# Kernel optimization log

Hardware: AMD Instinct MI355X
Metric: run time of the kernel (lower is better)

Reference implementation:

```python
import jax, jax.numpy as jnp
import numpy as np

HIDDEN = 2048
INTER = 768
N_EXPERTS = 64
TOP_K = 8
BATCH, SEQ = 2, 2048


def setup_inputs() -> dict:
    key = jax.random.key(0)
    k_x, k_g, k_gp, k_up, k_dp = jax.random.split(key, 5)
    s_in = 1.0 / np.sqrt(HIDDEN)   # lecun_normal fan_in scaling
    s_mid = 1.0 / np.sqrt(INTER)
    return {
        "x": jax.random.normal(k_x, (BATCH, SEQ, HIDDEN), dtype=jnp.float32),
        "gate_w": jax.random.normal(k_g, (HIDDEN, N_EXPERTS), dtype=jnp.float32) * s_in,
        "gate_proj": jax.random.normal(k_gp, (N_EXPERTS, HIDDEN, INTER), dtype=jnp.float32) * s_in,
        "up_proj": jax.random.normal(k_up, (N_EXPERTS, HIDDEN, INTER), dtype=jnp.float32) * s_in,
        "down_proj": jax.random.normal(k_dp, (N_EXPERTS, INTER, HIDDEN), dtype=jnp.float32) * s_mid,
    }


def reference(x, gate_w, gate_proj, up_proj, down_proj):
    H = x.shape[-1]
    E = gate_proj.shape[0]
    K = TOP_K

    x_flat = x.reshape(-1, H)                      # [T, H]
    router_logits = x_flat @ gate_w                # [T, E]

    routing_weights, selected_experts = jax.lax.top_k(router_logits, k=K)  # [T, K]
    routing_weights = jax.nn.softmax(routing_weights, axis=-1)

    sel_flat = jnp.ravel(selected_experts)         # [T*K]
    x_expanded = jnp.repeat(x_flat, K, axis=0)     # [T*K, H]

    sort_idx = jnp.argsort(sel_flat)
    unsort_idx = jnp.argsort(sort_idx)
    x_sorted = x_expanded[sort_idx]                # tokens grouped by expert
    group_sizes = jnp.bincount(sel_flat, length=E)

    gate_out = jax.lax.ragged_dot(x_sorted, gate_proj, group_sizes)  # [T*K, I]
    up_out = jax.lax.ragged_dot(x_sorted, up_proj, group_sizes)      # [T*K, I]
    activated = jax.nn.silu(gate_out) * up_out
    down_out = jax.lax.ragged_dot(activated, down_proj, group_sizes)  # [T*K, H]

    unsorted = down_out[unsort_idx].reshape(-1, K, H)  # [T, K, H]
    out = (unsorted * routing_weights[..., None]).sum(axis=1)
    return out.reshape(x.shape), router_logits
```

## Files before the change

kernel.cpp:

```cpp
#include <hip/hip_runtime.h>
#include <hip/hip_bf16.h>
#include <cstdint>

#define NTOK 4096
#define HID  2048
#define ITER 768
#define NEXP 64
#define TOPK 8
#define MAXT 320

typedef __attribute__((ext_vector_type(8))) short sh8;
typedef __attribute__((ext_vector_type(4))) float f32x4;

#define MFMA16 __builtin_amdgcn_mfma_f32_16x16x32_bf16

__device__ __forceinline__ uint16_t f2b(float f) {
  union { float f; uint32_t u; } v; v.f = f;
  uint32_t u = v.u;
  u += 0x7FFFu + ((u >> 16) & 1u);
  return (uint16_t)(u >> 16);
}

__device__ __forceinline__ float b2f_lo(uint32_t w) {
  union { uint32_t u; float f; } v; v.u = w << 16; return v.f;
}
__device__ __forceinline__ float b2f_hi(uint32_t w) {
  union { uint32_t u; float f; } v; v.u = w & 0xffff0000u; return v.f;
}

__device__ __forceinline__ uint32_t cvtpk(float lo, float hi) {
  float2 f2; f2.x = lo; f2.y = hi;
  __hip_bfloat162 h = __float22bfloat162_rn(f2);
  union { __hip_bfloat162 h; uint32_t u; } v; v.h = h;
  return v.u;
}

__device__ __forceinline__ void gl2lds16(const void* g, void* l) {
  __builtin_amdgcn_global_load_lds(
      (const __attribute__((address_space(1))) uint32_t*)g,
      (__attribute__((address_space(3))) uint32_t*)l, 16, 0, 0);
}

__device__ __forceinline__ int xcd_unswizzle(int s, int na) {
  int q = na >> 3, r = na & 7, x = s & 7, i = s >> 3;
  return (x < r ? x * (q + 1) : r * (q + 1) + (x - r) * q) + i;
}

__global__ void zero_kernel(int* __restrict__ cc) {
  cc[threadIdx.x] = 0;
}

__global__ __launch_bounds__(256) void xcast_kernel(const float* __restrict__ x,
                                                    uint16_t* __restrict__ xb) {
  size_t i = ((size_t)blockIdx.x * 256 + threadIdx.x) * 8;
  float4 a = *(const float4*)(x + i);
  float4 b = *(const float4*)(x + i + 4);
  uint4 o;
  o.x = (uint32_t)f2b(a.x) | ((uint32_t)f2b(a.y) << 16);
  o.y = (uint32_t)f2b(a.z) | ((uint32_t)f2b(a.w) << 16);
  o.z = (uint32_t)f2b(b.x) | ((uint32_t)f2b(b.y) << 16);
  o.w = (uint32_t)f2b(b.z) | ((uint32_t)f2b(b.w) << 16);
  *(uint4*)(xb + i) = o;
}

__global__ __launch_bounds__(256) void router_kernel(
    const float* __restrict__ x, const float* __restrict__ gate_w,
    float* __restrict__ logits, int* __restrict__ topk_id,
    float* __restrict__ topk_w, int* __restrict__ counts)
{
  int lane = threadIdx.x & 63;
  int wv   = threadIdx.x >> 6;
  int t    = blockIdx.x * 4 + wv;
  const float* xr = x + (size_t)t * HID;
  float acc = 0.f;
  #pragma unroll 4
  for (int h = 0; h < HID; h += 4) {
    float4 xv = *(const float4*)(xr + h);
    acc += xv.x * gate_w[(h + 0) * NEXP + lane];
    acc += xv.y * gate_w[(h + 1) * NEXP + lane];
    acc += xv.z * gate_w[(h + 2) * NEXP + lane];
    acc += xv.w * gate_w[(h + 3) * NEXP + lane];
  }
  logits[(size_t)t * NEXP + lane] = acc;

  float v = acc;
  float topv[TOPK]; int topi[TOPK];
  #pragma unroll
  for (int k = 0; k < TOPK; ++k) {
    float bv = v; int bi = lane;
    #pragma unroll
    for (int off = 32; off > 0; off >>= 1) {
      float ov = __shfl_xor(bv, off);
      int   oi = __shfl_xor(bi, off);
      if (ov > bv || (ov == bv && oi < bi)) { bv = ov; bi = oi; }
    }
    topv[k] = bv; topi[k] = bi;
    if (lane == bi) v = -3.0e38f;
  }
  float m = topv[0], s = 0.f, w[TOPK];
  #pragma unroll
  for (int k = 0; k < TOPK; ++k) { w[k] = __expf(topv[k] - m); s += w[k]; }
  float inv = 1.f / s;
  if (lane < TOPK) {
    topk_id[t * TOPK + lane] = topi[lane];
    topk_w[t * TOPK + lane]  = w[lane] * inv;
    atomicAdd(&counts[topi[lane]], 1);
  }
}

__global__ void offsets_kernel(const int* __restrict__ counts, int* __restrict__ offsets,
                               int* __restrict__ tiles, int* __restrict__ tilecount) {
  if (threadIdx.x == 0) {
    int s = 0, nt = 0;
    for (int e = 0; e < NEXP; ++e) {
      offsets[e] = s;
      int c = counts[e];
      for (int rb = 0; rb * 128 < c; ++rb) tiles[nt++] = (e << 16) | rb;
      s += c;
    }
    offsets[NEXP] = s;
    tilecount[0] = nt;
  }
}

__global__ __launch_bounds__(256) void scatter_kernel(
    const int* __restrict__ topk_id,
    const int* __restrict__ offsets, int* __restrict__ cursor,
    int* __restrict__ pair_tok, int* __restrict__ inv)
{
  int p = blockIdx.x * 256 + threadIdx.x;
  int e = topk_id[p];
  int pos = offsets[e] + atomicAdd(&cursor[e], 1);
  pair_tok[pos] = p;
  inv[p] = pos;
}

__global__ __launch_bounds__(256, 2) void gateup_kernel(
    const uint16_t* __restrict__ xb,
    const float* __restrict__ gate_proj,
    const float* __restrict__ up_proj,
    const int* __restrict__ pair_tok,
    const int* __restrict__ offsets,
    const int* __restrict__ tiles,
    const int* __restrict__ tilecount,
    uint16_t* __restrict__ act)
{
  const int nt = tilecount[0];
  const int na = nt * 12;
  if (blockIdx.x >= na) return;
  const int L  = xcd_unswizzle(blockIdx.x, na);
  const int ti = L % nt, nc = L / nt;
  const int te = tiles[ti];
  const int e = te >> 16, row0 = (te & 0xffff) * 128;
  const int start = offsets[e];
  const int count = offsets[e + 1] - start;
  const int nvalid = min(128, count - row0);

  __shared__ __align__(16) uint16_t aT[2 * 128 * 64];
  __shared__ __align__(16) uint16_t bT[128 * 64];
  __shared__ int s_tok[128];

  const int t = threadIdx.x, l = t & 63, w = t >> 6;
  if (t < 128)
    s_tok[t] = (t < nvalid) ? (pair_tok[start + row0 + t] >> 3) : 0;
  __syncthreads();

  const int sub = l >> 3;
  const int xk  = ((l & 7) ^ sub) << 3;
  const uint16_t* srcA[4]; char* dstA[4];
  #pragma unroll
  for (int q = 0; q < 4; ++q) {
    int rl = (w * 4 + q) * 8 + sub;
    srcA[q] = xb + (size_t)s_tok[rl] * HID + xk;
    dstA[q] = (char*)aT + (w * 4 + q) * 1024;
  }

  const int brow = t & 127;
  const int kk0  = (t >> 7) * 32;
  const int rcomb  = nc * 128 + brow;
  const int n_orig = ((rcomb >> 5) << 4) + (rcomb & 15);
  const int is_up  = (rcomb >> 4) & 1;
  const float* wsrc = (is_up ? up_proj : gate_proj)
                    + (size_t)e * HID * ITER + n_orig;
  uint16_t* bwr[4];
  #pragma unroll
  for (int s = 0; s < 4; ++s) {
    int kb = (kk0 * 2 + 16 * s) ^ ((brow & 7) << 4);
    bwr[s] = (uint16_t*)((char*)bT + brow * 128 + kb);
  }

  const int wr = w >> 1, wc = w & 1, lr = l & 15, hi = l >> 4;
  const int xorv = (lr & 7) << 4;

  f32x4 acc[4][4];
  #pragma unroll
  for (int mi = 0; mi < 4; ++mi)
    #pragma unroll
    for (int ni = 0; ni < 4; ++ni)
      acc[mi][ni] = (f32x4){0.f, 0.f, 0.f, 0.f};

  float va[32];
  {
    const float* wp = wsrc + (size_t)kk0 * ITER;
    #pragma unroll
    for (int j = 0; j < 32; ++j) va[j] = wp[(size_t)j * ITER];
  }
  #pragma unroll
  for (int q = 0; q < 4; ++q)
    gl2lds16(srcA[q], dstA[q]);

  for (int kc = 0; kc < 32; ++kc) {
    __syncthreads();
    #pragma unroll
    for (int s = 0; s < 4; ++s) {
      uint4 o;
      o.x = cvtpk(va[s * 8 + 0], va[s * 8 + 1]);
      o.y = cvtpk(va[s * 8 + 2], va[s * 8 + 3]);
      o.z = cvtpk(va[s * 8 + 4], va[s * 8 + 5]);
      o.w = cvtpk(va[s * 8 + 6], va[s * 8 + 7]);
      *(uint4*)bwr[s] = o;
    }
    __syncthreads();
    if (kc + 1 < 32) {
      const float* wp = wsrc + (size_t)((kc + 1) * 64 + kk0) * ITER;
      #pragma unroll
      for (int j = 0; j < 32; ++j) va[j] = wp[(size_t)j * ITER];
      #pragma unroll
      for (int q = 0; q < 4; ++q)
        gl2lds16(srcA[q] + (kc + 1) * 64, dstA[q] + ((kc + 1) & 1) * 16384);
    }
    __builtin_amdgcn_sched_barrier(0);
    const char* aBuf = (const char*)aT + (kc & 1) * 16384;
    #pragma unroll
    for (int ks = 0; ks < 2; ++ks) {
      sh8 af[4], bf[4];
      #pragma unroll
      for (int mi = 0; mi < 4; ++mi)
        af[mi] = *(const sh8*)(aBuf +
                   (wr * 64 + mi * 16 + lr) * 128 + ((ks * 64 + hi * 16) ^ xorv));
      #pragma unroll
      for (int ni = 0; ni < 4; ++ni)
        bf[ni] = *(const sh8*)((const char*)bT +
                   (wc * 64 + ni * 16 + lr) * 128 + ((ks * 64 + hi * 16) ^ xorv));
      #pragma unroll
      for (int mi = 0; mi < 4; ++mi)
        #pragma unroll
        for (int ni = 0; ni < 4; ++ni)
          acc[mi][ni] = MFMA16(af[mi], bf[ni], acc[mi][ni], 0, 0, 0);
    }
  }

  #pragma unroll
  for (int mi = 0; mi < 4; ++mi)
    #pragma unroll
    for (int p = 0; p < 2; ++p)
      #pragma unroll
      for (int j = 0; j < 4; ++j) {
        int row = wr * 64 + mi * 16 + hi * 4 + j;
        if (row < nvalid) {
          float g = acc[mi][2 * p][j], u = acc[mi][2 * p + 1][j];
          float a = (g / (1.f + __expf(-g))) * u;
          int col = nc * 64 + wc * 32 + p * 16 + lr;
          act[(size_t)(start + row0 + row) * ITER + col] = f2b(a);
        }
      }
}

__global__ __launch_bounds__(256, 2) void down_kernel(
    const uint16_t* __restrict__ act,
    const float* __restrict__ down_proj,
    const int* __restrict__ offsets,
    const int* __restrict__ tiles,
    const int* __restrict__ tilecount,
    uint16_t* __restrict__ dd)
{
  const int nt = tilecount[0];
  const int na = nt * 16;
  if (blockIdx.x >= na) return;
  const int L  = xcd_unswizzle(blockIdx.x, na);
  const int ti = L % nt, nc = L / nt;
  const int te = tiles[ti];
  const int e = te >> 16, row0 = (te & 0xffff) * 128;
  const int start = offsets[e];
  const int count = offsets[e + 1] - start;
  const int nvalid = min(128, count - row0);

  __shared__ __align__(16) uint16_t aT[2 * 128 * 64];
  __shared__ __align__(16) uint16_t bT[128 * 64];

  const int t = threadIdx.x, l = t & 63, w = t >> 6;

  const int sub = l >> 3;
  const int xk  = ((l & 7) ^ sub) << 3;

  const uint16_t* srcA[4]; char* dstA[4];
  #pragma unroll
  for (int q = 0; q < 4; ++q) {
    int rl = (w * 4 + q) * 8 + sub;
    srcA[q] = act + (size_t)(start + row0 + rl) * ITER + xk;
    dstA[q] = (char*)aT + (w * 4 + q) * 1024;
  }

  const int brow = t & 127;
  const int kk0  = (t >> 7) * 32;
  const float* wsrc = down_proj + (size_t)e * ITER * HID + nc * 128 + brow;
  uint16_t* bwr[4];
  #pragma unroll
  for (int s = 0; s < 4; ++s) {
    int kb = (kk0 * 2 + 16 * s) ^ ((brow & 7) << 4);
    bwr[s] = (uint16_t*)((char*)bT + brow * 128 + kb);
  }

  const int wr = w >> 1, wc = w & 1, lr = l & 15, hi = l >> 4;
  const int xorv = (lr & 7) << 4;

  f32x4 acc[4][4];
  #pragma unroll
  for (int mi = 0; mi < 4; ++mi)
    #pragma unroll
    for (int ni = 0; ni < 4; ++ni)
      acc[mi][ni] = (f32x4){0.f, 0.f, 0.f, 0.f};

  float va[32];
  {
    const float* wp = wsrc + (size_t)kk0 * HID;
    #pragma unroll
    for (int j = 0; j < 32; ++j) va[j] = wp[(size_t)j * HID];
  }
  #pragma unroll
  for (int q = 0; q < 4; ++q)
    gl2lds16(srcA[q], dstA[q]);

  for (int kc = 0; kc < 12; ++kc) {
    __syncthreads();
    #pragma unroll
    for (int s = 0; s < 4; ++s) {
      uint4 o;
      o.x = cvtpk(va[s * 8 + 0], va[s * 8 + 1]);
      o.y = cvtpk(va[s * 8 + 2], va[s * 8 + 3]);
      o.z = cvtpk(va[s * 8 + 4], va[s * 8 + 5]);
      o.w = cvtpk(va[s * 8 + 6], va[s * 8 + 7]);
      *(uint4*)bwr[s] = o;
    }
    __syncthreads();
    if (kc + 1 < 12) {
      const float* wp = wsrc + (size_t)((kc + 1) * 64 + kk0) * HID;
      #pragma unroll
      for (int j = 0; j < 32; ++j) va[j] = wp[(size_t)j * HID];
      #pragma unroll
      for (int q = 0; q < 4; ++q)
        gl2lds16(srcA[q] + (kc + 1) * 64, dstA[q] + ((kc + 1) & 1) * 16384);
    }
    __builtin_amdgcn_sched_barrier(0);
    const char* aBuf = (const char*)aT + (kc & 1) * 16384;
    #pragma unroll
    for (int ks = 0; ks < 2; ++ks) {
      sh8 af[4], bf[4];
      #pragma unroll
      for (int mi = 0; mi < 4; ++mi)
        af[mi] = *(const sh8*)(aBuf +
                   (wr * 64 + mi * 16 + lr) * 128 + ((ks * 64 + hi * 16) ^ xorv));
      #pragma unroll
      for (int ni = 0; ni < 4; ++ni)
        bf[ni] = *(const sh8*)((const char*)bT +
                   (wc * 64 + ni * 16 + lr) * 128 + ((ks * 64 + hi * 16) ^ xorv));
      #pragma unroll
      for (int mi = 0; mi < 4; ++mi)
        #pragma unroll
        for (int ni = 0; ni < 4; ++ni)
          acc[mi][ni] = MFMA16(af[mi], bf[ni], acc[mi][ni], 0, 0, 0);
    }
  }

  #pragma unroll
  for (int mi = 0; mi < 4; ++mi)
    #pragma unroll
    for (int ni = 0; ni < 4; ++ni)
      #pragma unroll
      for (int j = 0; j < 4; ++j) {
        int row = wr * 64 + mi * 16 + hi * 4 + j;
        if (row < nvalid) {
          int col = nc * 128 + wc * 64 + ni * 16 + lr;
          dd[(size_t)(start + row0 + row) * HID + col] = f2b(acc[mi][ni][j]);
        }
      }
}

__global__ __launch_bounds__(256) void reduce_kernel(
    const uint16_t* __restrict__ dd, const float* __restrict__ topk_w,
    const int* __restrict__ inv, float* __restrict__ out)
{
  const int tok = blockIdx.x;
  const int c   = threadIdx.x * 8;
  float acc[8] = {0.f, 0.f, 0.f, 0.f, 0.f, 0.f, 0.f, 0.f};
  #pragma unroll
  for (int k = 0; k < TOPK; ++k) {
    const int   pos = inv[tok * TOPK + k];
    const float wk  = topk_w[tok * TOPK + k];
    uint4 v = *(const uint4*)&dd[(size_t)pos * HID + c];
    acc[0] += wk * b2f_lo(v.x);  acc[1] += wk * b2f_hi(v.x);
    acc[2] += wk * b2f_lo(v.y);  acc[3] += wk * b2f_hi(v.y);
    acc[4] += wk * b2f_lo(v.z);  acc[5] += wk * b2f_hi(v.z);
    acc[6] += wk * b2f_lo(v.w);  acc[7] += wk * b2f_hi(v.w);
  }
  float4 o0 = {acc[0], acc[1], acc[2], acc[3]};
  float4 o1 = {acc[4], acc[5], acc[6], acc[7]};
  float* op = out + (size_t)tok * HID + c;
  *(float4*)op       = o0;
  *(float4*)(op + 4) = o1;
}

extern "C" void kernel_launch(void* const* d_in, const int* in_sizes, int n_in,
                              void* d_out, int out_size, void* d_ws, size_t ws_size,
                              hipStream_t stream) {
  const float* x         = (const float*)d_in[0];
  const float* gate_w    = (const float*)d_in[1];
  const float* gate_proj = (const float*)d_in[2];
  const float* up_proj   = (const float*)d_in[3];
  const float* down_proj = (const float*)d_in[4];

  float* out    = (float*)d_out;
  float* logits = out + (size_t)NTOK * HID;

  char* ws = (char*)d_ws;
  size_t off = 0;
  uint16_t* xb      = (uint16_t*)(ws + off); off += (size_t)NTOK * HID * 2;
  uint16_t* act     = (uint16_t*)(ws + off); off += (size_t)(NTOK * TOPK + 128) * ITER * 2;
  uint16_t* dd      = (uint16_t*)(ws + off); off += (size_t)(NTOK * TOPK + 128) * HID * 2;
  int*      topk_id = (int*)  (ws + off); off += (size_t)NTOK * TOPK * 4;
  float*    topk_w  = (float*)(ws + off); off += (size_t)NTOK * TOPK * 4;
  int*      counts  = (int*)  (ws + off); off += 256;
  int*      cursor  = (int*)  (ws + off); off += 256;
  int*      offsets = (int*)  (ws + off); off += 512;
  int*      tiles   = (int*)  (ws + off); off += MAXT * 4;
  int*      tilecount=(int*)  (ws + off); off += 256;
  int*      pair_tok= (int*)  (ws + off); off += (size_t)NTOK * TOPK * 4;
  int*      inv     = (int*)  (ws + off); off += (size_t)NTOK * TOPK * 4;

  zero_kernel   <<<1,    128, 0, stream>>>(counts);
  xcast_kernel  <<<4096, 256, 0, stream>>>(x, xb);
  router_kernel <<<1024, 256, 0, stream>>>(x, gate_w, logits, topk_id, topk_w, counts);
  offsets_kernel<<<1,    64,  0, stream>>>(counts, offsets, tiles, tilecount);
  scatter_kernel<<<128,  256, 0, stream>>>(topk_id, offsets, cursor, pair_tok, inv);

  gateup_kernel<<<MAXT * 12, 256, 0, stream>>>(xb, gate_proj, up_proj, pair_tok, offsets,
                                               tiles, tilecount, act);
  down_kernel  <<<MAXT * 16, 256, 0, stream>>>(act, down_proj, offsets,
                                               tiles, tilecount, dd);
  reduce_kernel<<<NTOK, 256, 0, stream>>>(dd, topk_w, inv, out);
}
```

Baseline: 889.6 us.

## Double-buffer weight tiles in LDS and pipeline loads two stages ahead

Both expert GEMM kernels now double-buffer the bf16 weight tile in LDS as well as the activation tile. The prologue preloads and converts stage 0 and prefetches stage 1 weights into registers. The main loop issues the next A tile, writes the converted next B tile, and starts global loads two stages ahead, then runs the MFMAs at raised priority. The two __syncthreads per iteration become one s_barrier with a partial vmcnt wait, so memory latency overlaps with compute. This doubles B-tile LDS use, which may lower occupancy, and the hand-written waitcnt must match the exact count of outstanding loads.

```diff
diff --git a/kernel.cpp b/kernel.cpp
--- a/kernel.cpp
+++ b/kernel.cpp
@@ -157,7 +157,7 @@
   const int nvalid = min(128, count - row0);
 
   __shared__ __align__(16) uint16_t aT[2 * 128 * 64];
-  __shared__ __align__(16) uint16_t bT[128 * 64];
+  __shared__ __align__(16) uint16_t bT[2 * 128 * 64];
   __shared__ int s_tok[128];
 
   const int t = threadIdx.x, l = t & 63, w = t >> 6;
@@ -201,16 +201,38 @@
 
   float va[32];
   {
-    const float* wp = wsrc + (size_t)kk0 * ITER;
-    #pragma unroll
-    for (int j = 0; j < 32; ++j) va[j] = wp[(size_t)j * ITER];
-  }
-  #pragma unroll
-  for (int q = 0; q < 4; ++q)
-    gl2lds16(srcA[q], dstA[q]);
+    const float* wp0 = wsrc + (size_t)kk0 * ITER;
+    float v0[32];
+    #pragma unroll
+    for (int j = 0; j < 32; ++j) v0[j] = wp0[(size_t)j * ITER];
+    #pragma unroll
+    for (int q = 0; q < 4; ++q) gl2lds16(srcA[q], dstA[q]);
+    __builtin_amdgcn_sched_barrier(0);
+    #pragma unroll
+    for (int s = 0; s < 4; ++s) {
+      uint4 o;
+      o.x = cvtpk(v0[s * 8 + 0], v0[s * 8 + 1]);
+      o.y = cvtpk(v0[s * 8 + 2], v0[s * 8 + 3]);
+      o.z = cvtpk(v0[s * 8 + 4], v0[s * 8 + 5]);
+      o.w = cvtpk(v0[s * 8 + 6], v0[s * 8 + 7]);
+      *(uint4*)bwr[s] = o;
+    }
+    __builtin_amdgcn_sched_barrier(0);
+    const float* wp1 = wsrc + (size_t)(64 + kk0) * ITER;
+    #pragma unroll
+    for (int j = 0; j < 32; ++j) va[j] = wp1[(size_t)j * ITER];
+    __builtin_amdgcn_sched_barrier(0);
+  }
+  asm volatile("s_waitcnt vmcnt(32) lgkmcnt(0)" ::: "memory");
+  __builtin_amdgcn_s_barrier();
 
   for (int kc = 0; kc < 32; ++kc) {
-    __syncthreads();
+    const int cur = kc & 1, nxt = cur ^ 1;
+    const int k1 = min(kc + 1, 31);
+    #pragma unroll
+    for (int q = 0; q < 4; ++q)
+      gl2lds16(srcA[q] + k1 * 64, dstA[q] + nxt * 16384);
+    __builtin_amdgcn_sched_barrier(0);
     #pragma unroll
     for (int s = 0; s < 4; ++s) {
       uint4 o;
@@ -218,19 +240,19 @@
       o.y = cvtpk(va[s * 8 + 2], va[s * 8 + 3]);
       o.z = cvtpk(va[s * 8 + 4], va[s * 8 + 5]);
       o.w = cvtpk(va[s * 8 + 6], va[s * 8 + 7]);
-      *(uint4*)bwr[s] = o;
-    }
-    __syncthreads();
-    if (kc + 1 < 32) {
-      const float* wp = wsrc + (size_t)((kc + 1) * 64 + kk0) * ITER;
+      *(uint4*)(bwr[s] + nxt * 8192) = o;
+    }
+    __builtin_amdgcn_sched_barrier(0);
+    const int k2 = min(kc + 2, 31);
+    {
+      const float* wp = wsrc + (size_t)(k2 * 64 + kk0) * ITER;
       #pragma unroll
       for (int j = 0; j < 32; ++j) va[j] = wp[(size_t)j * ITER];
-      #pragma unroll
-      for (int q = 0; q < 4; ++q)
-        gl2lds16(srcA[q] + (kc + 1) * 64, dstA[q] + ((kc + 1) & 1) * 16384);
-    }
-    __builtin_amdgcn_sched_barrier(0);
-    const char* aBuf = (const char*)aT + (kc & 1) * 16384;
+    }
+    __builtin_amdgcn_sched_barrier(0);
+    __builtin_amdgcn_s_setprio(1);
+    const char* aBuf = (const char*)aT + cur * 16384;
+    const char* bBuf = (const char*)bT + cur * 16384;
     #pragma unroll
     for (int ks = 0; ks < 2; ++ks) {
       sh8 af[4], bf[4];
@@ -240,7 +262,7 @@
                    (wr * 64 + mi * 16 + lr) * 128 + ((ks * 64 + hi * 16) ^ xorv));
       #pragma unroll
       for (int ni = 0; ni < 4; ++ni)
-        bf[ni] = *(const sh8*)((const char*)bT +
+        bf[ni] = *(const sh8*)(bBuf +
                    (wc * 64 + ni * 16 + lr) * 128 + ((ks * 64 + hi * 16) ^ xorv));
       #pragma unroll
       for (int mi = 0; mi < 4; ++mi)
@@ -248,6 +270,10 @@
         for (int ni = 0; ni < 4; ++ni)
           acc[mi][ni] = MFMA16(af[mi], bf[ni], acc[mi][ni], 0, 0, 0);
     }
+    __builtin_amdgcn_s_setprio(0);
+    __builtin_amdgcn_sched_barrier(0);
+    asm volatile("s_waitcnt vmcnt(32) lgkmcnt(0)" ::: "memory");
+    __builtin_amdgcn_s_barrier();
   }
 
   #pragma unroll
@@ -286,7 +312,7 @@
   const int nvalid = min(128, count - row0);
 
   __shared__ __align__(16) uint16_t aT[2 * 128 * 64];
-  __shared__ __align__(16) uint16_t bT[128 * 64];
+  __shared__ __align__(16) uint16_t bT[2 * 128 * 64];
 
   const int t = threadIdx.x, l = t & 63, w = t >> 6;
 
@@ -323,16 +349,38 @@
 
   float va[32];
   {
-    const float* wp = wsrc + (size_t)kk0 * HID;
-    #pragma unroll
-    for (int j = 0; j < 32; ++j) va[j] = wp[(size_t)j * HID];
-  }
-  #pragma unroll
-  for (int q = 0; q < 4; ++q)
-    gl2lds16(srcA[q], dstA[q]);
+    const float* wp0 = wsrc + (size_t)kk0 * HID;
+    float v0[32];
+    #pragma unroll
+    for (int j = 0; j < 32; ++j) v0[j] = wp0[(size_t)j * HID];
+    #pragma unroll
+    for (int q = 0; q < 4; ++q) gl2lds16(srcA[q], dstA[q]);
+    __builtin_amdgcn_sched_barrier(0);
+    #pragma unroll
+    for (int s = 0; s < 4; ++s) {
+      uint4 o;
+      o.x = cvtpk(v0[s * 8 + 0], v0[s * 8 + 1]);
+      o.y = cvtpk(v0[s * 8 + 2], v0[s * 8 + 3]);
+      o.z = cvtpk(v0[s * 8 + 4], v0[s * 8 + 5]);
+      o.w = cvtpk(v0[s * 8 + 6], v0[s * 8 + 7]);
+      *(uint4*)bwr[s] = o;
+    }
+    __builtin_amdgcn_sched_barrier(0);
+    const float* wp1 = wsrc + (size_t)(64 + kk0) * HID;
+    #pragma unroll
+    for (int j = 0; j < 32; ++j) va[j] = wp1[(size_t)j * HID];
+    __builtin_amdgcn_sched_barrier(0);
+  }
+  asm volatile("s_waitcnt vmcnt(32) lgkmcnt(0)" ::: "memory");
+  __builtin_amdgcn_s_barrier();
 
   for (int kc = 0; kc < 12; ++kc) {
-    __syncthreads();
+    const int cur = kc & 1, nxt = cur ^ 1;
+    const int k1 = min(kc + 1, 11);
+    #pragma unroll
+    for (int q = 0; q < 4; ++q)
+      gl2lds16(srcA[q] + k1 * 64, dstA[q] + nxt * 16384);
+    __builtin_amdgcn_sched_barrier(0);
     #pragma unroll
     for (int s = 0; s < 4; ++s) {
       uint4 o;
@@ -340,19 +388,19 @@
       o.y = cvtpk(va[s * 8 + 2], va[s * 8 + 3]);
       o.z = cvtpk(va[s * 8 + 4], va[s * 8 + 5]);
       o.w = cvtpk(va[s * 8 + 6], va[s * 8 + 7]);
-      *(uint4*)bwr[s] = o;
-    }
-    __syncthreads();
-    if (kc + 1 < 12) {
-      const float* wp = wsrc + (size_t)((kc + 1) * 64 + kk0) * HID;
+      *(uint4*)(bwr[s] + nxt * 8192) = o;
+    }
+    __builtin_amdgcn_sched_barrier(0);
+    const int k2 = min(kc + 2, 11);
+    {
+      const float* wp = wsrc + (size_t)(k2 * 64 + kk0) * HID;
       #pragma unroll
       for (int j = 0; j < 32; ++j) va[j] = wp[(size_t)j * HID];
-      #pragma unroll
-      for (int q = 0; q < 4; ++q)
-        gl2lds16(srcA[q] + (kc + 1) * 64, dstA[q] + ((kc + 1) & 1) * 16384);
-    }
-    __builtin_amdgcn_sched_barrier(0);
-    const char* aBuf = (const char*)aT + (kc & 1) * 16384;
+    }
+    __builtin_amdgcn_sched_barrier(0);
+    __builtin_amdgcn_s_setprio(1);
+    const char* aBuf = (const char*)aT + cur * 16384;
+    const char* bBuf = (const char*)bT + cur * 16384;
     #pragma unroll
     for (int ks = 0; ks < 2; ++ks) {
       sh8 af[4], bf[4];
@@ -362,7 +410,7 @@
                    (wr * 64 + mi * 16 + lr) * 128 + ((ks * 64 + hi * 16) ^ xorv));
       #pragma unroll
       for (int ni = 0; ni < 4; ++ni)
-        bf[ni] = *(const sh8*)((const char*)bT +
+        bf[ni] = *(const sh8*)(bBuf +
                    (wc * 64 + ni * 16 + lr) * 128 + ((ks * 64 + hi * 16) ^ xorv));
       #pragma unroll
       for (int mi = 0; mi < 4; ++mi)
@@ -370,6 +418,10 @@
         for (int ni = 0; ni < 4; ++ni)
           acc[mi][ni] = MFMA16(af[mi], bf[ni], acc[mi][ni], 0, 0, 0);
     }
+    __builtin_amdgcn_s_setprio(0);
+    __builtin_amdgcn_sched_barrier(0);
+    asm volatile("s_waitcnt vmcnt(32) lgkmcnt(0)" ::: "memory");
+    __builtin_amdgcn_s_barrier();
   }
 
   #pragma unroll
```

Result: slower. 977.2 us (+9.9%).
